# Optimization experiments

Hardware: AMD Instinct MI355X
Metric: run time of the kernel (lower is better)

## Reference

```python
import jax, jax.numpy as jnp
import numpy as np

DIM = 256
NH = 8
KA = 3
DR = 4
CR = DIM // DR            # 64 reduced dim
CPH = CR // NH            # 8 channels per head
SCALE = (DIM // NH) ** -0.5  # head_dim uses full dim, per original code


def _unfold_kernel():
    # fixed identity depthwise kernel: out channel c*KA*KA+i picks window offset i of channel c
    eye = jnp.eye(KA * KA, dtype=jnp.float32).reshape(KA * KA, 1, KA, KA)
    return jnp.tile(eye, (CPH, 1, 1, 1))  # (KA*KA*CPH, 1, KA, KA)


def _dwconv(x, w, b):
    # x: (N, CPH, H, W), w: (KA*KA*CPH, 1, KA, KA), groups=CPH, 'same' zero padding
    y = jax.lax.conv_general_dilated(
        x, w, window_strides=(1, 1), padding=[(KA // 2, KA // 2)] * 2,
        dimension_numbers=("NCHW", "OIHW", "NCHW"), feature_group_count=CPH)
    return y + b[None, :, None, None]


def setup_inputs() -> dict:
    key = jax.random.key(0)
    ks = jax.random.split(key, 8)
    B, L = 16, 4096
    x = jax.random.normal(ks[0], (B, L, DIM), dtype=jnp.float32)
    qkv_w = jax.random.normal(ks[1], (3 * CR, DIM), dtype=jnp.float32) * 0.02
    qkv_b = jnp.zeros((3 * CR,), dtype=jnp.float32)
    dep_conv_b = jax.random.normal(ks[2], (KA * KA * CPH,), dtype=jnp.float32) * 0.02
    dep_conv1_w = jax.random.normal(ks[3], (KA * KA * CPH, 1, KA, KA), dtype=jnp.float32) * 0.02
    dep_conv1_b = jnp.zeros((KA * KA * CPH,), dtype=jnp.float32)
    rpb_table = jax.random.normal(ks[4], (1, NH, 1, KA * KA, 1, 1), dtype=jnp.float32) * 0.02
    proj_w = jax.random.normal(ks[5], (DIM, CR), dtype=jnp.float32) * 0.02
    proj_b = jnp.zeros((DIM,), dtype=jnp.float32)
    return {
        "x": x, "H22": 64, "W22": 64,
        "relative_pos_index": jax.random.randint(ks[6], (9, 9), 0, 9),
        "relative_coords_table": jax.random.normal(ks[7], (9, 2), dtype=jnp.float32),
        "qkv_w": qkv_w, "qkv_b": qkv_b,
        "dep_conv_b": dep_conv_b, "dep_conv1_w": dep_conv1_w, "dep_conv1_b": dep_conv1_b,
        "rpb_table": rpb_table, "proj_w": proj_w, "proj_b": proj_b,
    }


def reference(x, H22, W22, relative_pos_index, relative_coords_table,
              qkv_w, qkv_b, dep_conv_b, dep_conv1_w, dep_conv1_b,
              rpb_table, proj_w, proj_b):
    B1, L1, C1 = x.shape
    H = int(np.sqrt(L1)); W = H
    # faithful to original: reshape (B,L,C)->(B,C,H,W) then move channels last
    xhw = x.reshape(B1, C1, H, W).transpose(0, 2, 3, 1)       # (B,H,W,C)
    qkv = xhw @ qkv_w.T + qkv_b                               # (B,H,W,3*CR)
    f = qkv.transpose(0, 3, 1, 2).reshape(B1 * NH, 3 * CPH, H, W)
    q = (f[:, :CPH] * SCALE).reshape(B1, NH, CPH, 1, H, W)
    kk = f[:, CPH:2 * CPH]                                    # (B*NH, CPH, H, W)
    vv = f[:, 2 * CPH:]
    w0 = _unfold_kernel()
    k = _dwconv(kk, w0, dep_conv_b) + _dwconv(kk, dep_conv1_w, dep_conv1_b)
    v = _dwconv(vv, w0, dep_conv_b) + _dwconv(vv, dep_conv1_w, dep_conv1_b)
    k = k.reshape(B1, NH, CPH, KA * KA, H, W) + rpb_table     # rpb bias on k
    v = v.reshape(B1, NH, CPH, KA * KA, H, W)
    attn = jax.nn.softmax((q * k).sum(2, keepdims=True), axis=3)  # (B,NH,1,ka*ka,H,W)
    out = (attn * v).sum(3).reshape(B1, CR, H, W).transpose(0, 2, 3, 1)  # (B,H,W,CR)
    out = out @ proj_w.T + proj_b                              # (B,H,W,C1)
    return out.transpose(0, 3, 1, 2).reshape(B1, L1, C1)
```

## Files before the change

kernel.cpp:

```cpp
#include <hip/hip_runtime.h>

#define BB 16
#define HW 4096
#define DIMC 256
#define NHEAD 8
#define CPH 8
#define NQKV 192
#define SCALE 0.17677669529663687f

typedef __attribute__((ext_vector_type(8))) short bf16x8;
typedef __attribute__((ext_vector_type(4))) float f32x4;

__device__ inline unsigned short f2b(float f) {
  union { float f; unsigned int u; } x; x.f = f;
  unsigned int r = x.u + 0x7FFFu + ((x.u >> 16) & 1u);
  return (unsigned short)(r >> 16);
}
__device__ inline float b2f(unsigned short u) {
  union { unsigned int u; float f; } x; x.u = ((unsigned int)u) << 16;
  return x.f;
}

__global__ __launch_bounds__(256) void cast_all(const float* __restrict__ qw,
                                                unsigned short* __restrict__ qwf,
                                                const float* __restrict__ dcb,
                                                const float* __restrict__ w1,
                                                const float* __restrict__ dc1b,
                                                const float* __restrict__ rpb,
                                                float* __restrict__ prep,
                                                const float* __restrict__ pw,
                                                unsigned short* __restrict__ pwf) {
  if (blockIdx.x == 24) {
    for (int e = threadIdx.x; e < 1056; e += 256) {
      float v = 0.f;
      if (e < 864) {
        int cp = e / 12, rs = e - cp * 12;
        if (rs < 9) v = w1[cp * 9 + rs] + ((cp % 9) == rs ? 1.f : 0.f);
      } else if (e < 960) {
        int i = e - 864; int c = i / 12, p = i - c * 12;
        if (p < 9) v = dcb[c * 9 + p] + dc1b[c * 9 + p];
      } else {
        int i = e - 960; int n = i / 12, p = i - n * 12;
        if (p < 9) v = rpb[n * 9 + p];
      }
      prep[e] = v;
    }
    return;
  }
  if (blockIdx.x >= 25) {
    int t = (blockIdx.x - 25) * 256 + threadIdx.x;
    int lane = t & 63;
    int cell = t >> 6;
    int m = lane & 15, g = lane >> 4;
    int band = cell >> 1, c32 = cell & 1;
    int d = band * 16 + m;
    int j = c32 * 32 + g * 8;
    unsigned short pk[8];
#pragma unroll
    for (int i = 0; i < 8; ++i) pk[i] = f2b(pw[d * 64 + j + i]);
    *(uint4*)&pwf[(size_t)t * 8] = *(uint4*)pk;
    return;
  }
  int t = blockIdx.x * 256 + threadIdx.x;
  int lane = t & 63;
  int cell = t >> 6;
  int m = lane & 15, g = lane >> 4;
  int band = cell >> 3, c32 = cell & 7;
  int j = band * 16 + m;
  int k = c32 * 32 + g * 8;
  unsigned short pk[8];
#pragma unroll
  for (int i = 0; i < 8; ++i) pk[i] = f2b(qw[j * 256 + k + i]);
  *(uint4*)&qwf[(size_t)t * 8] = *(uint4*)pk;
}

__global__ __launch_bounds__(256) void qkv_mfma(const float* __restrict__ x,
                                                const unsigned short* __restrict__ qwf,
                                                const float* __restrict__ qb,
                                                unsigned short* __restrict__ qkvt) {
  __shared__ unsigned short Bs[128 * 256];
  const int b = blockIdx.y;
  const int s_blk = blockIdx.x * 128;
  const int tid = threadIdx.x;
  const int wave = tid >> 6, lane = tid & 63;
  const float* xb = x + (size_t)b * (DIMC * HW);

  {
    const int s_row = (wave & 1) * 64 + lane;
    const int k_base = (wave >> 1) * 128;
    const float* p = xb + (size_t)k_base * HW + s_blk + s_row;
#pragma unroll
    for (int kc = 0; kc < 16; ++kc) {
      unsigned short pk[8];
#pragma unroll
      for (int j = 0; j < 8; ++j) {
        pk[j] = f2b(*p);
        p += HW;
      }
      int mc = (k_base >> 3) + kc;
      int stc = (mc & 24) | ((mc ^ s_row) & 7);
      *(uint4*)&Bs[s_row * 256 + stc * 8] = *(uint4*)pk;
    }
  }
  __syncthreads();

  f32x4 acc[3][8];
#pragma unroll
  for (int t = 0; t < 3; ++t)
#pragma unroll
    for (int st = 0; st < 8; ++st) acc[t][st] = (f32x4){0.f, 0.f, 0.f, 0.f};

  const int n = lane & 15, g = lane >> 4;
#pragma unroll
  for (int c32 = 0; c32 < 8; ++c32) {
    bf16x8 af[3];
#pragma unroll
    for (int t = 0; t < 3; ++t) {
      int band = wave * 3 + t;
      af[t] = *(const bf16x8*)(qwf + ((size_t)(band * 8 + c32) * 64 + lane) * 8);
    }
#pragma unroll
    for (int st = 0; st < 8; ++st) {
      int s_row = st * 16 + n;
      int mc = c32 * 4 + g;
      int stc = (mc & 24) | ((mc ^ s_row) & 7);
      bf16x8 bf = *(const bf16x8*)&Bs[s_row * 256 + stc * 8];
#pragma unroll
      for (int t = 0; t < 3; ++t)
        acc[t][st] = __builtin_amdgcn_mfma_f32_16x16x32_bf16(af[t], bf, acc[t][st], 0, 0, 0);
    }
  }

  unsigned short* ob = qkvt + (size_t)b * (NQKV * HW);
#pragma unroll
  for (int t = 0; t < 3; ++t) {
    int j0 = (wave * 3 + t) * 16 + g * 4;
#pragma unroll
    for (int st = 0; st < 8; ++st) {
      int s = s_blk + st * 16 + n;
#pragma unroll
      for (int r = 0; r < 4; ++r) {
        float v = acc[t][st][r] + qb[j0 + r];
        ob[(size_t)(j0 + r) * HW + s] = f2b(v);
      }
    }
  }
}

__global__ __launch_bounds__(512, 4) void attn_proj(const unsigned short* __restrict__ qkvt,
                                                    const float* __restrict__ prep,
                                                    const unsigned short* __restrict__ pwf,
                                                    const float* __restrict__ pb,
                                                    float* __restrict__ out) {
  __shared__ float hal[16][6][20];
  __shared__ __align__(16) float wA[8][108];
  __shared__ float Kbs[8][8][12];
  __shared__ float Vbs[8][12];
  __shared__ float Qs[8][68];
  __shared__ unsigned short Ao[64][64];

  const int b = blockIdx.x;
  const int ty = blockIdx.y;
  const int h0 = (ty >> 2) * 4, w0 = (ty & 3) * 16;
  const int tid = threadIdx.x;
  const int w = tid >> 6, lane = tid & 63;
  const int c = lane & 7;
  const int pi = lane >> 3;
  const int pidx = w * 8 + pi;
  const int pr = pidx >> 4, pc = pidx & 15;
  const unsigned short* fbase = qkvt + (size_t)b * (NQKV * HW);

  for (int e = tid; e < 864; e += 512) ((float*)wA)[e] = prep[e];
  if (tid < 96) {
    int cc = tid / 12, p = tid - cc * 12;
    Vbs[cc][p] = prep[864 + tid];
  }
  for (int e = tid; e < 768; e += 512) {
    int nn = e / 96, r = e - nn * 96;
    int p = r % 12;
    Kbs[nn][r / 12][p] = prep[864 + r] + prep[960 + nn * 12 + p];
  }

  for (int n = 0; n < 8; ++n) {
    const unsigned short* fb = fbase + (size_t)n * 24 * HW;
    __syncthreads();

    {
      int cq = tid >> 6, px = tid & 63;
      int sp = (h0 + (px >> 4)) * 64 + w0 + (px & 15);
      Qs[cq][px] = SCALE * b2f(fb[(size_t)cq * HW + sp]);
    }
    for (int e = tid; e < 1728; e += 512) {
      int cb = e / 108;
      int rem = e - cb * 108;
      int y = rem / 18, xx = rem - y * 18;
      int gy = h0 - 1 + y, gx = w0 - 1 + xx;
      float v = 0.f;
      if ((unsigned)gy < 64u && (unsigned)gx < 64u)
        v = b2f(fb[(size_t)(8 + cb) * HW + gy * 64 + gx]);
      hal[cb][y][xx] = v;
    }
    __syncthreads();

    const float* wAc = &wA[c][0];
    const float qc = Qs[c][pidx];
    const float* Kbn = &Kbs[n][c][0];

    float ax[9];
    {
      float t[9];
#pragma unroll
      for (int dy = 0; dy < 3; ++dy)
#pragma unroll
        for (int dx = 0; dx < 3; ++dx)
          t[dy * 3 + dx] = hal[c][pr + dy][pc + dx];
#pragma unroll
      for (int p = 0; p < 9; ++p) {
        float kx = Kbn[p];
#pragma unroll
        for (int rs = 0; rs < 9; ++rs)
          kx = fmaf(wAc[p * 12 + rs], t[rs], kx);
        float lx = qc * kx;
        lx += __shfl_xor(lx, 1);
        lx += __shfl_xor(lx, 2);
        lx += __shfl_xor(lx, 4);
        ax[p] = lx;
      }
    }

    {
      float mx = -1e30f;
#pragma unroll
      for (int p = 0; p < 9; ++p) mx = fmaxf(mx, ax[p]);
      float dx = 0.f;
#pragma unroll
      for (int p = 0; p < 9; ++p) { ax[p] = __expf(ax[p] - mx); dx += ax[p]; }
      float ix = 1.f / dx;
#pragma unroll
      for (int p = 0; p < 9; ++p) ax[p] *= ix;
    }

    {
      float t[9];
#pragma unroll
      for (int dy = 0; dy < 3; ++dy)
#pragma unroll
        for (int dx = 0; dx < 3; ++dx)
          t[dy * 3 + dx] = hal[8 + c][pr + dy][pc + dx];
      float oc = 0.f;
#pragma unroll
      for (int p = 0; p < 9; ++p) {
        float vx = Vbs[c][p];
#pragma unroll
        for (int rs = 0; rs < 9; ++rs)
          vx = fmaf(wAc[p * 12 + rs], t[rs], vx);
        oc = fmaf(ax[p], vx, oc);
      }
      Ao[pidx][((n ^ (pidx & 7)) << 3) + c] = f2b(oc);
    }
  }
  __syncthreads();

  f32x4 acc[2][4];
#pragma unroll
  for (int t = 0; t < 2; ++t)
#pragma unroll
    for (int st = 0; st < 4; ++st) acc[t][st] = (f32x4){0.f, 0.f, 0.f, 0.f};

  const int nn = lane & 15, g = lane >> 4;
#pragma unroll
  for (int c32 = 0; c32 < 2; ++c32) {
    bf16x8 af[2];
#pragma unroll
    for (int t = 0; t < 2; ++t) {
      int band = w * 2 + t;
      af[t] = *(const bf16x8*)(pwf + ((size_t)(band * 2 + c32) * 64 + lane) * 8);
    }
#pragma unroll
    for (int st = 0; st < 4; ++st) {
      int s_row = st * 16 + nn;
      int stc = (c32 * 4 + g) ^ (s_row & 7);
      bf16x8 bf = *(const bf16x8*)&Ao[s_row][stc * 8];
#pragma unroll
      for (int t = 0; t < 2; ++t)
        acc[t][st] = __builtin_amdgcn_mfma_f32_16x16x32_bf16(af[t], bf, acc[t][st], 0, 0, 0);
    }
  }

  float bias[2][4];
#pragma unroll
  for (int t = 0; t < 2; ++t)
#pragma unroll
    for (int r = 0; r < 4; ++r) bias[t][r] = pb[(w * 2 + t) * 16 + g * 4 + r];

  float* ob = out + ((size_t)b << 20);
#pragma unroll
  for (int t = 0; t < 2; ++t) {
    int d0 = (w * 2 + t) * 16 + g * 4;
#pragma unroll
    for (int st = 0; st < 4; ++st) {
      int sp = (h0 + st) * 64 + w0 + nn;
#pragma unroll
      for (int r = 0; r < 4; ++r)
        ob[(size_t)(d0 + r) * HW + sp] = acc[t][st][r] + bias[t][r];
    }
  }
}

extern "C" void kernel_launch(void* const* d_in, const int* in_sizes, int n_in,
                              void* d_out, int out_size, void* d_ws, size_t ws_size,
                              hipStream_t stream) {
  (void)in_sizes; (void)n_in; (void)out_size; (void)ws_size;
  const float* x    = (const float*)d_in[0];
  const float* qw   = (const float*)d_in[5];
  const float* qb   = (const float*)d_in[6];
  const float* dcb  = (const float*)d_in[7];
  const float* w1   = (const float*)d_in[8];
  const float* dc1b = (const float*)d_in[9];
  const float* rpb  = (const float*)d_in[10];
  const float* pw   = (const float*)d_in[11];
  const float* pb   = (const float*)d_in[12];

  unsigned short* qkvt = (unsigned short*)d_ws;
  unsigned short* qwf  = (unsigned short*)((char*)d_ws + 25165824);
  float* prep          = (float*)((char*)d_ws + 29360128);
  unsigned short* pwf  = (unsigned short*)((char*)d_ws + 30408704);

  cast_all<<<33, 256, 0, stream>>>(qw, qwf, dcb, w1, dc1b, rpb, prep, pw, pwf);
  qkv_mfma<<<dim3(32, BB), 256, 0, stream>>>(x, qwf, qb, qkvt);
  attn_proj<<<dim3(BB, 64), 512, 0, stream>>>(qkvt, prep, pwf, pb, (float*)d_out);
}
```

Before: 207.0 us.

## Register-block attention over 2x2 pixels, prefetch next head halo, enlarge tile

The attention+projection kernel now covers an 8x16 pixel tile with 256 threads, and each thread computes a 2x2 pixel block so the 4x4 halo window and the 81 conv weights (now held in registers) are reused across four outputs. Each head's halo and Q values are loaded into registers one iteration ahead, overlapping global loads with compute. The projection MFMA stage grows to 4x8 tiles per wave. The intent is to cut LDS traffic and per-pixel weight reads and to hide load latency, at the cost of high register pressure (A[81], ax[4][9], acc[4][8]) and half as many blocks.

```diff
diff --git a/kernel.cpp b/kernel.cpp
--- a/kernel.cpp
+++ b/kernel.cpp
@@ -147,158 +147,212 @@
   }
 }
 
-__global__ __launch_bounds__(512, 4) void attn_proj(const unsigned short* __restrict__ qkvt,
+__global__ __launch_bounds__(256, 2) void attn_proj(const unsigned short* __restrict__ qkvt,
                                                     const float* __restrict__ prep,
                                                     const unsigned short* __restrict__ pwf,
                                                     const float* __restrict__ pb,
                                                     float* __restrict__ out) {
-  __shared__ float hal[16][6][20];
-  __shared__ __align__(16) float wA[8][108];
-  __shared__ float Kbs[8][8][12];
-  __shared__ float Vbs[8][12];
-  __shared__ float Qs[8][68];
-  __shared__ unsigned short Ao[64][64];
+  __shared__ float hal[2880];
+  __shared__ float Rbs[96];
+  __shared__ unsigned short Ao[128][64];
 
   const int b = blockIdx.x;
   const int ty = blockIdx.y;
-  const int h0 = (ty >> 2) * 4, w0 = (ty & 3) * 16;
+  const int h0 = (ty >> 2) * 8, w0 = (ty & 3) * 16;
   const int tid = threadIdx.x;
-  const int w = tid >> 6, lane = tid & 63;
-  const int c = lane & 7;
-  const int pi = lane >> 3;
-  const int pidx = w * 8 + pi;
-  const int pr = pidx >> 4, pc = pidx & 15;
+  const int w = tid >> 6;
+  const int c = tid & 7;
+  const int qk = (tid >> 3) & 7;
   const unsigned short* fbase = qkvt + (size_t)b * (NQKV * HW);
 
-  for (int e = tid; e < 864; e += 512) ((float*)wA)[e] = prep[e];
-  if (tid < 96) {
-    int cc = tid / 12, p = tid - cc * 12;
-    Vbs[cc][p] = prep[864 + tid];
-  }
-  for (int e = tid; e < 768; e += 512) {
-    int nn = e / 96, r = e - nn * 96;
-    int p = r % 12;
-    Kbs[nn][r / 12][p] = prep[864 + r] + prep[960 + nn * 12 + p];
-  }
+  if (tid < 96) Rbs[tid] = prep[960 + tid];
+
+  float A[81];
+  {
+    const float* ap = prep + c * 108;
+#pragma unroll
+    for (int p = 0; p < 9; ++p) {
+      float4 a0 = *(const float4*)(ap + p * 12);
+      float4 a1 = *(const float4*)(ap + p * 12 + 4);
+      A[p*9+0]=a0.x; A[p*9+1]=a0.y; A[p*9+2]=a0.z; A[p*9+3]=a0.w;
+      A[p*9+4]=a1.x; A[p*9+5]=a1.y; A[p*9+6]=a1.z; A[p*9+7]=a1.w;
+      A[p*9+8]=ap[p*12+8];
+    }
+  }
+  float Vb[9];
+#pragma unroll
+  for (int p = 0; p < 9; ++p) Vb[p] = prep[864 + c * 12 + p];
+
+  int hofs[12];
+#pragma unroll
+  for (int i = 0; i < 12; ++i) {
+    int e = tid + i * 256;
+    int cb = e / 180;
+    int rem = e - cb * 180;
+    int y = rem / 18, xx = rem - y * 18;
+    int gy = h0 - 1 + y, gx = w0 - 1 + xx;
+    bool ok = (e < 2880) && ((unsigned)gy < 64u) && ((unsigned)gx < 64u);
+    hofs[i] = ok ? ((8 + cb) * HW + gy * 64 + gx) : -1;
+  }
+  int gq[4];
+#pragma unroll
+  for (int dy = 0; dy < 2; ++dy)
+#pragma unroll
+    for (int dx = 0; dx < 2; ++dx)
+      gq[dy * 2 + dx] = c * HW + (h0 + 2 * w + dy) * 64 + w0 + 2 * qk + dx;
+
+  unsigned short hreg[12], qreg[4];
+  {
+    const unsigned short* fb = fbase;
+#pragma unroll
+    for (int i = 0; i < 12; ++i) hreg[i] = fb[hofs[i] < 0 ? 0 : hofs[i]];
+#pragma unroll
+    for (int i = 0; i < 4; ++i) qreg[i] = fb[gq[i]];
+  }
+
+  const int tbase = c * 180 + w * 36 + qk * 2;
 
   for (int n = 0; n < 8; ++n) {
-    const unsigned short* fb = fbase + (size_t)n * 24 * HW;
     __syncthreads();
-
+#pragma unroll
+    for (int i = 0; i < 11; ++i)
+      hal[tid + i * 256] = (hofs[i] >= 0) ? b2f(hreg[i]) : 0.f;
+    if (tid < 64) hal[tid + 11 * 256] = (hofs[11] >= 0) ? b2f(hreg[11]) : 0.f;
+    float qc[4];
+#pragma unroll
+    for (int i = 0; i < 4; ++i) qc[i] = SCALE * b2f(qreg[i]);
+    if (n < 7) {
+      const unsigned short* f2 = fbase + (size_t)(n + 1) * 24 * HW;
+#pragma unroll
+      for (int i = 0; i < 12; ++i) hreg[i] = f2[hofs[i] < 0 ? 0 : hofs[i]];
+#pragma unroll
+      for (int i = 0; i < 4; ++i) qreg[i] = f2[gq[i]];
+    }
+    __syncthreads();
+
+    float Kb[9];
+#pragma unroll
+    for (int p = 0; p < 9; ++p) Kb[p] = Vb[p] + Rbs[n * 12 + p];
+
+    float ax[4][9];
     {
-      int cq = tid >> 6, px = tid & 63;
-      int sp = (h0 + (px >> 4)) * 64 + w0 + (px & 15);
-      Qs[cq][px] = SCALE * b2f(fb[(size_t)cq * HW + sp]);
-    }
-    for (int e = tid; e < 1728; e += 512) {
-      int cb = e / 108;
-      int rem = e - cb * 108;
-      int y = rem / 18, xx = rem - y * 18;
-      int gy = h0 - 1 + y, gx = w0 - 1 + xx;
-      float v = 0.f;
-      if ((unsigned)gy < 64u && (unsigned)gx < 64u)
-        v = b2f(fb[(size_t)(8 + cb) * HW + gy * 64 + gx]);
-      hal[cb][y][xx] = v;
-    }
-    __syncthreads();
-
-    const float* wAc = &wA[c][0];
-    const float qc = Qs[c][pidx];
-    const float* Kbn = &Kbs[n][c][0];
-
-    float ax[9];
+      float t[16];
+#pragma unroll
+      for (int i = 0; i < 4; ++i)
+#pragma unroll
+        for (int j = 0; j < 4; ++j)
+          t[i * 4 + j] = hal[tbase + i * 18 + j];
+#pragma unroll
+      for (int p = 0; p < 9; ++p) {
+        float k0 = Kb[p], k1 = Kb[p], k2 = Kb[p], k3 = Kb[p];
+#pragma unroll
+        for (int ry = 0; ry < 3; ++ry)
+#pragma unroll
+          for (int rx = 0; rx < 3; ++rx) {
+            float a = A[p * 9 + ry * 3 + rx];
+            k0 = fmaf(a, t[ry * 4 + rx],           k0);
+            k1 = fmaf(a, t[ry * 4 + rx + 1],       k1);
+            k2 = fmaf(a, t[(ry + 1) * 4 + rx],     k2);
+            k3 = fmaf(a, t[(ry + 1) * 4 + rx + 1], k3);
+          }
+        float l0 = qc[0] * k0, l1 = qc[1] * k1, l2 = qc[2] * k2, l3 = qc[3] * k3;
+        l0 += __shfl_xor(l0, 1); l1 += __shfl_xor(l1, 1); l2 += __shfl_xor(l2, 1); l3 += __shfl_xor(l3, 1);
+        l0 += __shfl_xor(l0, 2); l1 += __shfl_xor(l1, 2); l2 += __shfl_xor(l2, 2); l3 += __shfl_xor(l3, 2);
+        l0 += __shfl_xor(l0, 4); l1 += __shfl_xor(l1, 4); l2 += __shfl_xor(l2, 4); l3 += __shfl_xor(l3, 4);
+        ax[0][p] = l0; ax[1][p] = l1; ax[2][p] = l2; ax[3][p] = l3;
+      }
+    }
+
+#pragma unroll
+    for (int i = 0; i < 4; ++i) {
+      float mx = -1e30f;
+#pragma unroll
+      for (int p = 0; p < 9; ++p) mx = fmaxf(mx, ax[i][p]);
+      float dx = 0.f;
+#pragma unroll
+      for (int p = 0; p < 9; ++p) { ax[i][p] = __expf(ax[i][p] - mx); dx += ax[i][p]; }
+      float ix = 1.f / dx;
+#pragma unroll
+      for (int p = 0; p < 9; ++p) ax[i][p] *= ix;
+    }
+
     {
-      float t[9];
-#pragma unroll
-      for (int dy = 0; dy < 3; ++dy)
-#pragma unroll
-        for (int dx = 0; dx < 3; ++dx)
-          t[dy * 3 + dx] = hal[c][pr + dy][pc + dx];
+      float t[16];
+#pragma unroll
+      for (int i = 0; i < 4; ++i)
+#pragma unroll
+        for (int j = 0; j < 4; ++j)
+          t[i * 4 + j] = hal[tbase + 1440 + i * 18 + j];
+      float o0 = 0.f, o1 = 0.f, o2 = 0.f, o3 = 0.f;
 #pragma unroll
       for (int p = 0; p < 9; ++p) {
-        float kx = Kbn[p];
-#pragma unroll
-        for (int rs = 0; rs < 9; ++rs)
-          kx = fmaf(wAc[p * 12 + rs], t[rs], kx);
-        float lx = qc * kx;
-        lx += __shfl_xor(lx, 1);
-        lx += __shfl_xor(lx, 2);
-        lx += __shfl_xor(lx, 4);
-        ax[p] = lx;
-      }
-    }
-
-    {
-      float mx = -1e30f;
-#pragma unroll
-      for (int p = 0; p < 9; ++p) mx = fmaxf(mx, ax[p]);
-      float dx = 0.f;
-#pragma unroll
-      for (int p = 0; p < 9; ++p) { ax[p] = __expf(ax[p] - mx); dx += ax[p]; }
-      float ix = 1.f / dx;
-#pragma unroll
-      for (int p = 0; p < 9; ++p) ax[p] *= ix;
-    }
-
-    {
-      float t[9];
-#pragma unroll
-      for (int dy = 0; dy < 3; ++dy)
-#pragma unroll
-        for (int dx = 0; dx < 3; ++dx)
-          t[dy * 3 + dx] = hal[8 + c][pr + dy][pc + dx];
-      float oc = 0.f;
-#pragma unroll
-      for (int p = 0; p < 9; ++p) {
-        float vx = Vbs[c][p];
-#pragma unroll
-        for (int rs = 0; rs < 9; ++rs)
-          vx = fmaf(wAc[p * 12 + rs], t[rs], vx);
-        oc = fmaf(ax[p], vx, oc);
-      }
-      Ao[pidx][((n ^ (pidx & 7)) << 3) + c] = f2b(oc);
+        float v0 = Vb[p], v1 = Vb[p], v2 = Vb[p], v3 = Vb[p];
+#pragma unroll
+        for (int ry = 0; ry < 3; ++ry)
+#pragma unroll
+          for (int rx = 0; rx < 3; ++rx) {
+            float a = A[p * 9 + ry * 3 + rx];
+            v0 = fmaf(a, t[ry * 4 + rx],           v0);
+            v1 = fmaf(a, t[ry * 4 + rx + 1],       v1);
+            v2 = fmaf(a, t[(ry + 1) * 4 + rx],     v2);
+            v3 = fmaf(a, t[(ry + 1) * 4 + rx + 1], v3);
+          }
+        o0 = fmaf(ax[0][p], v0, o0);
+        o1 = fmaf(ax[1][p], v1, o1);
+        o2 = fmaf(ax[2][p], v2, o2);
+        o3 = fmaf(ax[3][p], v3, o3);
+      }
+      int px0 = (2 * w) * 16 + 2 * qk;
+      int px1 = px0 + 1;
+      int px2 = px0 + 16;
+      int px3 = px0 + 17;
+      Ao[px0][((n ^ (px0 & 7)) << 3) + c] = f2b(o0);
+      Ao[px1][((n ^ (px1 & 7)) << 3) + c] = f2b(o1);
+      Ao[px2][((n ^ (px2 & 7)) << 3) + c] = f2b(o2);
+      Ao[px3][((n ^ (px3 & 7)) << 3) + c] = f2b(o3);
     }
   }
   __syncthreads();
 
-  f32x4 acc[2][4];
-#pragma unroll
-  for (int t = 0; t < 2; ++t)
-#pragma unroll
-    for (int st = 0; st < 4; ++st) acc[t][st] = (f32x4){0.f, 0.f, 0.f, 0.f};
+  const int lane = tid & 63;
+  f32x4 acc[4][8];
+#pragma unroll
+  for (int t = 0; t < 4; ++t)
+#pragma unroll
+    for (int st = 0; st < 8; ++st) acc[t][st] = (f32x4){0.f, 0.f, 0.f, 0.f};
 
   const int nn = lane & 15, g = lane >> 4;
 #pragma unroll
   for (int c32 = 0; c32 < 2; ++c32) {
-    bf16x8 af[2];
-#pragma unroll
-    for (int t = 0; t < 2; ++t) {
-      int band = w * 2 + t;
+    bf16x8 af[4];
+#pragma unroll
+    for (int t = 0; t < 4; ++t) {
+      int band = w * 4 + t;
       af[t] = *(const bf16x8*)(pwf + ((size_t)(band * 2 + c32) * 64 + lane) * 8);
     }
 #pragma unroll
-    for (int st = 0; st < 4; ++st) {
+    for (int st = 0; st < 8; ++st) {
       int s_row = st * 16 + nn;
       int stc = (c32 * 4 + g) ^ (s_row & 7);
       bf16x8 bf = *(const bf16x8*)&Ao[s_row][stc * 8];
 #pragma unroll
-      for (int t = 0; t < 2; ++t)
+      for (int t = 0; t < 4; ++t)
         acc[t][st] = __builtin_amdgcn_mfma_f32_16x16x32_bf16(af[t], bf, acc[t][st], 0, 0, 0);
     }
   }
 
-  float bias[2][4];
-#pragma unroll
-  for (int t = 0; t < 2; ++t)
-#pragma unroll
-    for (int r = 0; r < 4; ++r) bias[t][r] = pb[(w * 2 + t) * 16 + g * 4 + r];
+  float bias[4][4];
+#pragma unroll
+  for (int t = 0; t < 4; ++t)
+#pragma unroll
+    for (int r = 0; r < 4; ++r) bias[t][r] = pb[(w * 4 + t) * 16 + g * 4 + r];
 
   float* ob = out + ((size_t)b << 20);
 #pragma unroll
-  for (int t = 0; t < 2; ++t) {
-    int d0 = (w * 2 + t) * 16 + g * 4;
-#pragma unroll
-    for (int st = 0; st < 4; ++st) {
+  for (int t = 0; t < 4; ++t) {
+    int d0 = (w * 4 + t) * 16 + g * 4;
+#pragma unroll
+    for (int st = 0; st < 8; ++st) {
       int sp = (h0 + st) * 64 + w0 + nn;
 #pragma unroll
       for (int r = 0; r < 4; ++r)
@@ -328,5 +382,5 @@
 
   cast_all<<<33, 256, 0, stream>>>(qw, qwf, dcb, w1, dc1b, rpb, prep, pw, pwf);
   qkv_mfma<<<dim3(32, BB), 256, 0, stream>>>(x, qwf, qb, qkvt);
-  attn_proj<<<dim3(BB, 64), 512, 0, stream>>>(qkvt, prep, pwf, pb, (float*)d_out);
-}
+  attn_proj<<<dim3(BB, 32), 256, 0, stream>>>(qkvt, prep, pwf, pb, (float*)d_out);
+}
```

Measured after the change: 182.1 us. -12.1%, faster.
